# Performance work log

Measured on AMD Instinct MI355X. Metric: run time of the kernel, lower is better.

The kernel has to match this reference:

```python
import jax, jax.numpy as jnp
import numpy as np

N, E, D = 50000, 200000, 128   # graph nodes, graph edges (= line-graph nodes), feature dim
L = 2                          # number of GINEConv iterations (linegraph init arg)


def _build_line_graph(col0, col1):
    """Exact sparse equivalent of torch.nonzero((col1[:,None]==col0[None,:]) & (col0[:,None]!=col1[:,None])).
    Returns line edges (i -> j) with col1[i] == col0[j] and edge i not a self-loop,
    plus edge_attr_idx = col1[lg_src] (the shared graph node)."""
    order = np.argsort(col0, kind='stable')              # edges grouped by source node
    counts = np.bincount(col0, minlength=N)              # out-degree per node
    offsets = np.concatenate([[0], np.cumsum(counts)[:-1]])
    lengths = np.where(col0 != col1, counts[col1], 0)    # successors of each non-self-loop edge
    M = int(lengths.sum())
    lg_src = np.repeat(np.arange(E), lengths)
    cum = np.cumsum(lengths)
    pos = np.arange(M) - np.repeat(cum - lengths, lengths)  # position within each successor block
    lg_dst = order[np.repeat(offsets[col1], lengths) + pos]
    edge_attr_idx = col1[lg_src]
    return lg_src.astype(np.int64), lg_dst.astype(np.int64), edge_attr_idx.astype(np.int64)


def setup_inputs() -> dict:
    rng = np.random.RandomState(0)
    col0 = rng.randint(0, N, size=E).astype(np.int64)
    col1 = rng.randint(0, N, size=E).astype(np.int64)
    lg_src, lg_dst, edge_attr_idx = _build_line_graph(col0, col1)

    key = jax.random.key(0)
    kx, k1, k2 = jax.random.split(key, 3)
    scale = (2.0 / D) ** 0.5
    return {
        'x':  jax.random.normal(kx, (N, D), dtype=jnp.float32),
        'W1': jax.random.normal(k1, (D, D), dtype=jnp.float32) * scale,
        'b1': jnp.zeros((D,), dtype=jnp.float32),
        'W2': jax.random.normal(k2, (D, D), dtype=jnp.float32) * scale,
        'b2': jnp.zeros((D,), dtype=jnp.float32),
        'col0': jnp.asarray(col0),
        'col1': jnp.asarray(col1),
        'lg_src': jnp.asarray(lg_src),
        'lg_dst': jnp.asarray(lg_dst),
        'edge_attr_idx': jnp.asarray(edge_attr_idx),
    }


def reference(x, W1, b1, W2, b2, col0, col1, lg_src, lg_dst, edge_attr_idx):
    # line-graph node features: mean of endpoint features of each original edge
    lgX = 0.5 * (x[col0] + x[col1])                       # [E, D]
    lgE = x[edge_attr_idx]                                # [M, D] line-edge attrs (fixed across iterations)

    for _ in range(L):  # GINEConv, eps = 0 (PyG default)
        m = jax.nn.relu(lgX[lg_src] + lgE)                # [M, D] messages
        aggr = jax.ops.segment_sum(m, lg_dst, num_segments=E)  # scatter-add at target line-nodes
        h = lgX + aggr                                    # (1 + eps) * x + aggr
        lgX = jax.nn.relu(h @ W1 + b1) @ W2 + b2          # gin_nn MLP

    # scatter_mean back to graph nodes by col1 (zeros where no incident edge, matching pad)
    sums = jax.ops.segment_sum(lgX, col1, num_segments=N)                     # [N, D]
    cnt = jax.ops.segment_sum(jnp.ones((lgX.shape[0], 1), lgX.dtype), col1, num_segments=N)
    gx = jnp.where(cnt > 0, sums / jnp.maximum(cnt, 1.0), 0.0)

    out = jax.nn.relu(gx)
    # dropout p=0.0 -> identity; residual=True
    return x + out
```

## Files before the change

### kernel.cpp

```cpp
#include <hip/hip_runtime.h>
#include <hip/hip_bf16.h>

constexpr int NN = 50000;
constexpr int EE = 200000;
typedef __bf16 bf16x8 __attribute__((ext_vector_type(8)));
typedef float f32x4 __attribute__((ext_vector_type(4)));

__device__ __forceinline__ float b2f(unsigned short s) {
    union { unsigned u; float f; } c; c.u = ((unsigned)s) << 16; return c.f;
}
__device__ __forceinline__ unsigned short f2b(float f) {
    union { float f; unsigned u; } c; c.f = f;
    unsigned u = c.u + 0x7fffu + ((c.u >> 16) & 1u);
    return (unsigned short)(u >> 16);
}
__device__ __forceinline__ float xv(const void* p, long i, int f32m) {
    return f32m ? ((const float*)p)[i] : b2f(((const unsigned short*)p)[i]);
}
__device__ __forceinline__ int iv(const int* p, int i, int i64m) {
    return i64m ? p[2 * i] : p[i];
}

__global__ void k_detect(const unsigned short* x16, const int* c32, int* flg) {
    __shared__ int sf, si;
    int t = threadIdx.x;
    if (t == 0) { sf = 0; si = 1; }
    __syncthreads();
    for (int i = t; i < 16384; i += 256)
        if (((x16[i] >> 7) & 0xFF) == 0xFF) sf = 1;
    if (t < 64)
        if (c32[2 * t + 1] != 0) si = 0;
    __syncthreads();
    if (t == 0) { flg[0] = sf; flg[1] = si; }
}

__global__ void k_zero(unsigned* p, int n) {
    int i = blockIdx.x * 256 + threadIdx.x;
    if (i < n) p[i] = 0u;
}

__global__ void k_cast(const void* x, unsigned short* xb, const int* flg) {
    int i = blockIdx.x * 256 + threadIdx.x;
    if (i >= NN * 16) return;
    if (flg[0]) {
        const float4* xp = (const float4*)x + (size_t)i * 2;
        float4 u = xp[0], v = xp[1];
        unsigned short o[8] = { f2b(u.x), f2b(u.y), f2b(u.z), f2b(u.w),
                                f2b(v.x), f2b(v.y), f2b(v.z), f2b(v.w) };
        *(uint4*)(xb + (size_t)i * 8) = *(const uint4*)o;
    } else {
        ((uint4*)xb)[i] = ((const uint4*)x)[i];
    }
}

__global__ void k_wfrag(const void* W, unsigned short* Wf, const int* flg) {
    int f32m = flg[0];
    int chunk = blockIdx.x * 256 + threadIdx.x;
    if (chunk >= 2048) return;
    int l = chunk & 63, c = (chunk >> 6) & 3, t = chunk >> 8;
    int n = t * 16 + (l & 15), k0 = c * 32 + ((l >> 4) * 8);
    for (int j = 0; j < 8; j++) Wf[chunk * 8 + j] = f2b(xv(W, (long)(k0 + j) * 128 + n, f32m));
}

__global__ void k_hist(const int* col1, int* counts, const int* flg) {
    int e = blockIdx.x * 256 + threadIdx.x;
    if (e >= EE) return;
    atomicAdd(&counts[iv(col1, e, flg[1])], 1);
}

__global__ void k_scan1(const int* counts, int* bsum) {
    __shared__ int sh[256];
    int b = blockIdx.x, t = threadIdx.x;
    int idx = b * 256 + t;
    sh[t] = (idx < NN) ? counts[idx] : 0;
    __syncthreads();
    for (int off = 128; off > 0; off >>= 1) {
        if (t < off) sh[t] += sh[t + off];
        __syncthreads();
    }
    if (t == 0) bsum[b] = sh[0];
}

__global__ void k_scan2(const int* counts, const int* bsum,
                        int* row_ptr, int* cursor) {
    __shared__ int sh[256];
    __shared__ int base_s;
    int b = blockIdx.x, t = threadIdx.x;
    sh[t] = (t < b) ? bsum[t] : 0;
    __syncthreads();
    for (int off = 128; off > 0; off >>= 1) {
        if (t < off) sh[t] += sh[t + off];
        __syncthreads();
    }
    if (t == 0) base_s = sh[0];
    __syncthreads();
    int idx = b * 256 + t;
    int v = (idx < NN) ? counts[idx] : 0;
    sh[t] = v;
    __syncthreads();
    for (int off = 1; off < 256; off <<= 1) {
        int add = (t >= off) ? sh[t - off] : 0;
        __syncthreads();
        sh[t] += add;
        __syncthreads();
    }
    int ex = base_s + sh[t] - v;
    if (idx < NN) { row_ptr[idx] = ex; cursor[idx] = ex; }
    if (idx == NN - 1) row_ptr[NN] = ex + v;
}

__global__ void k_cscatter(const int* col0, const int* col1, int* cursor,
                           unsigned* aux, int* node1, const int* flg) {
    int e = blockIdx.x * 256 + threadIdx.x;
    if (e >= EE) return;
    int i64m = flg[1];
    int a = iv(col0, e, i64m), b = iv(col1, e, i64m);
    int pos = atomicAdd(&cursor[b], 1);
    aux[pos] = (unsigned)a | (a == b ? 0x80000000u : 0u);
    node1[pos] = b;
}

__global__ void k_gath(const unsigned short* xb, const unsigned short* lgX,
                       const int* row_ptr, const unsigned* aux,
                       unsigned short* S, int mode) {
    int n = blockIdx.x * 4 + (threadIdx.x >> 6);
    if (n >= NN) return;
    int l = threadIdx.x & 63, k0 = l * 2;
    int lo = row_ptr[n], hi = row_ptr[n + 1];
    unsigned un = *(const unsigned*)(xb + (size_t)n * 128 + k0);
    float xn0 = b2f((unsigned short)un), xn1 = b2f((unsigned short)(un >> 16));
    float a0 = 0.0f, a1 = 0.0f;
    if (mode == 1) {
        for (int p = lo; p < hi; p++) {
            unsigned av = aux[p];
            if (av & 0x80000000u) continue;
            unsigned u = *(const unsigned*)(xb + (size_t)av * 128 + k0);
            a0 += fmaxf(0.5f * b2f((unsigned short)u) + 1.5f * xn0, 0.0f);
            a1 += fmaxf(0.5f * b2f((unsigned short)(u >> 16)) + 1.5f * xn1, 0.0f);
        }
    } else {
        for (int p = lo; p < hi; p++) {
            if (aux[p] & 0x80000000u) continue;
            unsigned u = *(const unsigned*)(lgX + (size_t)p * 128 + k0);
            a0 += fmaxf(b2f((unsigned short)u) + xn0, 0.0f);
            a1 += fmaxf(b2f((unsigned short)(u >> 16)) + xn1, 0.0f);
        }
    }
    unsigned o = ((unsigned)f2b(a1) << 16) | (unsigned)f2b(a0);
    *(unsigned*)(S + (size_t)n * 128 + k0) = o;
}

__global__ __launch_bounds__(256, 8)
void k_fused(const unsigned short* A, const unsigned short* S,
             const unsigned* aux, const int* node1, const unsigned short* xb,
             const void* bias1, const void* bias2,
             const unsigned short* Wf1, const unsigned short* Wf2,
             unsigned short* Out, const int* flg, int initA) {
    __shared__ unsigned short Lds[8192];
    int f32m = flg[0];
    int tid = threadIdx.x;
    int w = tid >> 6, l = tid & 63;
    int lq = l >> 4, ln = l & 15;
    int e0 = blockIdx.x * 64 + w * 16;
    unsigned short* W_ = Lds + w * 2048;

    int row = e0 + ln;
    int aN = (int)(aux[row] & 0x7fffffffu);
    int bN = initA ? node1[row] : 0;
    for (int c = 0; c < 4; c++) {
        int k0 = c * 32 + lq * 8;
        uint4 svv = *(const uint4*)(S + (size_t)aN * 128 + k0);
        const unsigned short* sp = (const unsigned short*)&svv;
        unsigned short v[8];
        if (initA) {
            uint4 xav = *(const uint4*)(xb + (size_t)aN * 128 + k0);
            uint4 xbv = *(const uint4*)(xb + (size_t)bN * 128 + k0);
            const unsigned short* xa = (const unsigned short*)&xav;
            const unsigned short* xc = (const unsigned short*)&xbv;
            for (int j = 0; j < 8; j++)
                v[j] = f2b(0.5f * (b2f(xa[j]) + b2f(xc[j])) + b2f(sp[j]));
        } else {
            uint4 av = *(const uint4*)(A + (size_t)row * 128 + k0);
            const unsigned short* ap = (const unsigned short*)&av;
            for (int j = 0; j < 8; j++) v[j] = f2b(b2f(ap[j]) + b2f(sp[j]));
        }
        *(uint4*)(W_ + (c * 64 + l) * 8) = *(const uint4*)v;
    }

    f32x4 acc[8];
    for (int j = 0; j < 8; j++)
        for (int r = 0; r < 4; r++) acc[j][r] = 0.0f;
    for (int c = 0; c < 4; c++) {
        bf16x8 af = *(const bf16x8*)(W_ + (c * 64 + l) * 8);
        for (int j = 0; j < 8; j++) {
            bf16x8 bf = *(const bf16x8*)(Wf1 + (size_t)(((j * 4 + c) * 64 + l) * 8));
            acc[j] = __builtin_amdgcn_mfma_f32_16x16x32_bf16(af, bf, acc[j], 0, 0, 0);
        }
    }

    for (int j = 0; j < 8; j++) {
        int n = j * 16 + ln;
        float bv = xv(bias1, n, f32m);
        int c2 = n >> 5, lhi = ((n >> 3) & 3) * 16, j2 = n & 7;
        for (int rg = 0; rg < 4; rg++) {
            float h = acc[j][rg] + bv;
            if (h < 0.0f) h = 0.0f;
            W_[(c2 * 64 + lhi + lq * 4 + rg) * 8 + j2] = f2b(h);
        }
    }

    for (int j = 0; j < 8; j++)
        for (int r = 0; r < 4; r++) acc[j][r] = 0.0f;
    for (int c = 0; c < 4; c++) {
        bf16x8 af = *(const bf16x8*)(W_ + (c * 64 + l) * 8);
        for (int j = 0; j < 8; j++) {
            bf16x8 bf = *(const bf16x8*)(Wf2 + (size_t)(((j * 4 + c) * 64 + l) * 8));
            acc[j] = __builtin_amdgcn_mfma_f32_16x16x32_bf16(af, bf, acc[j], 0, 0, 0);
        }
    }

    for (int j = 0; j < 8; j++) {
        int n = j * 16 + ln;
        float bv = xv(bias2, n, f32m);
        for (int rg = 0; rg < 4; rg++)
            W_[(lq * 4 + rg) * 128 + n] = f2b(acc[j][rg] + bv);
    }
    for (int i = 0; i < 4; i++) {
        int idx = i * 64 + l;
        ((uint4*)Out)[(size_t)e0 * 16 + idx] = ((const uint4*)W_)[idx];
    }
}

__global__ void LGNNGINELayer_12463995093126_kernel(
    const void* x, const unsigned short* lgX, const int* row_ptr,
    void* out, const int* flg) {
    int n = blockIdx.x * 4 + (threadIdx.x >> 6);
    if (n >= NN) return;
    int l = threadIdx.x & 63, k0 = l * 2;
    int f32m = flg[0];
    int lo = row_ptr[n], hi = row_ptr[n + 1];
    float a0 = 0.0f, a1 = 0.0f;
    for (int p = lo; p < hi; p++) {
        unsigned u = *(const unsigned*)(lgX + (size_t)p * 128 + k0);
        a0 += b2f((unsigned short)u);
        a1 += b2f((unsigned short)(u >> 16));
    }
    float g0 = 0.0f, g1 = 0.0f;
    if (hi > lo) {
        float inv = 1.0f / (float)(hi - lo);
        g0 = fmaxf(a0 * inv, 0.0f);
        g1 = fmaxf(a1 * inv, 0.0f);
    }
    if (f32m) {
        ((float*)out)[(long)n * 128 + k0]     = ((const float*)x)[(long)n * 128 + k0] + g0;
        ((float*)out)[(long)n * 128 + k0 + 1] = ((const float*)x)[(long)n * 128 + k0 + 1] + g1;
    } else {
        unsigned u = *(const unsigned*)((const unsigned short*)x + (long)n * 128 + k0);
        float r0 = b2f((unsigned short)u) + g0;
        float r1 = b2f((unsigned short)(u >> 16)) + g1;
        unsigned o = ((unsigned)f2b(r1) << 16) | (unsigned)f2b(r0);
        *(unsigned*)((unsigned short*)out + (long)n * 128 + k0) = o;
    }
}

extern "C" void kernel_launch(void* const* d_in, const int* in_sizes, int n_in,
                              void* d_out, int out_size, void* d_ws, size_t ws_size,
                              hipStream_t stream) {
    (void)in_sizes; (void)n_in; (void)out_size; (void)ws_size;
    const void* x = d_in[0];
    const void* W1 = d_in[1];
    const void* b1 = d_in[2];
    const void* W2 = d_in[3];
    const void* b2 = d_in[4];
    const int* col0 = (const int*)d_in[5];
    const int* col1 = (const int*)d_in[6];

    char* p = (char*)d_ws;
    unsigned short* lgX = (unsigned short*)p; p += (size_t)EE * 128 * 2;
    unsigned short* S = (unsigned short*)p;   p += (size_t)NN * 128 * 2;
    unsigned short* xb = (unsigned short*)p;  p += (size_t)NN * 128 * 2;
    int* row_ptr = (int*)p;                   p += (size_t)(NN + 16) * 4;
    int* cursor = (int*)p;                    p += (size_t)NN * 4;
    int* counts = (int*)p;                    p += (size_t)NN * 4;
    int* bsum = (int*)p;                      p += 256 * 4;
    unsigned* aux = (unsigned*)p;             p += (size_t)EE * 4;
    int* node1 = (int*)p;                     p += (size_t)EE * 4;
    int* flg = (int*)p;                       p += 256;
    unsigned short* Wf1 = (unsigned short*)p; p += 16384 * 2;
    unsigned short* Wf2 = (unsigned short*)p;

    int gB = EE / 64;
    int eB = (EE + 255) / 256;
    int nB4 = (NN + 3) / 4;
    int sB = (NN + 255) / 256;
    int cB = (NN * 16 + 255) / 256;

    k_detect<<<1, 256, 0, stream>>>((const unsigned short*)x, col0, flg);
    k_cast<<<cB, 256, 0, stream>>>(x, xb, flg);
    k_wfrag<<<8, 256, 0, stream>>>(W1, Wf1, flg);
    k_wfrag<<<8, 256, 0, stream>>>(W2, Wf2, flg);

    k_zero<<<(NN + 255) / 256, 256, 0, stream>>>((unsigned*)counts, NN);
    k_hist<<<eB, 256, 0, stream>>>(col1, counts, flg);
    k_scan1<<<sB, 256, 0, stream>>>(counts, bsum);
    k_scan2<<<sB, 256, 0, stream>>>(counts, bsum, row_ptr, cursor);
    k_cscatter<<<eB, 256, 0, stream>>>(col0, col1, cursor, aux, node1, flg);

    k_gath<<<nB4, 256, 0, stream>>>(xb, lgX, row_ptr, aux, S, 1);
    k_fused<<<gB, 256, 0, stream>>>(lgX, S, aux, node1, xb, b1, b2,
                                    Wf1, Wf2, lgX, flg, 1);
    k_gath<<<nB4, 256, 0, stream>>>(xb, lgX, row_ptr, aux, S, 2);
    k_fused<<<gB, 256, 0, stream>>>(lgX, S, aux, node1, xb, b1, b2,
                                    Wf1, Wf2, lgX, flg, 0);
    LGNNGINELayer_12463995093126_kernel<<<nB4, 256, 0, stream>>>(
        x, lgX, row_ptr, d_out, flg);
}
```

Baseline: 383.0 us.

## Use hardware bf16 conversion, merge weight-fragment launches, keep A operand in registers

Replaces the manual round-to-nearest bf16 packing with native __bf16 casts and packed stores in several kernels. The two weight-fragment launches become one 16-block launch, and the counts zero kernel becomes hipMemsetAsync. In the fused MLP kernel the first GEMM's A fragments stay in registers instead of going through an LDS store and reload. These trim launch count and conversion instructions, at the cost of somewhat higher register pressure in the fused kernel.

```diff
diff --git a/kernel.cpp b/kernel.cpp
--- a/kernel.cpp
+++ b/kernel.cpp
@@ -9,6 +9,12 @@
 __device__ __forceinline__ float b2f(unsigned short s) {
     union { unsigned u; float f; } c; c.u = ((unsigned)s) << 16; return c.f;
 }
+__device__ __forceinline__ unsigned short bfbits(float f) {
+    union { __bf16 b; unsigned short u; } c; c.b = (__bf16)f; return c.u;
+}
+__device__ __forceinline__ unsigned pkbf(float lo, float hi) {
+    return ((unsigned)bfbits(hi) << 16) | bfbits(lo);
+}
 __device__ __forceinline__ unsigned short f2b(float f) {
     union { float f; unsigned u; } c; c.f = f;
     unsigned u = c.u + 0x7fffu + ((c.u >> 16) & 1u);
@@ -32,11 +38,6 @@
         if (c32[2 * t + 1] != 0) si = 0;
     __syncthreads();
     if (t == 0) { flg[0] = sf; flg[1] = si; }
-}
-
-__global__ void k_zero(unsigned* p, int n) {
-    int i = blockIdx.x * 256 + threadIdx.x;
-    if (i < n) p[i] = 0u;
 }
 
 __global__ void k_cast(const void* x, unsigned short* xb, const int* flg) {
@@ -45,21 +46,25 @@
     if (flg[0]) {
         const float4* xp = (const float4*)x + (size_t)i * 2;
         float4 u = xp[0], v = xp[1];
-        unsigned short o[8] = { f2b(u.x), f2b(u.y), f2b(u.z), f2b(u.w),
-                                f2b(v.x), f2b(v.y), f2b(v.z), f2b(v.w) };
-        *(uint4*)(xb + (size_t)i * 8) = *(const uint4*)o;
+        uint4 o;
+        o.x = pkbf(u.x, u.y); o.y = pkbf(u.z, u.w);
+        o.z = pkbf(v.x, v.y); o.w = pkbf(v.z, v.w);
+        ((uint4*)xb)[i] = o;
     } else {
         ((uint4*)xb)[i] = ((const uint4*)x)[i];
     }
 }
 
-__global__ void k_wfrag(const void* W, unsigned short* Wf, const int* flg) {
+__global__ void k_wfrag2(const void* W1, const void* W2,
+                         unsigned short* Wf1, unsigned short* Wf2, const int* flg) {
     int f32m = flg[0];
-    int chunk = blockIdx.x * 256 + threadIdx.x;
-    if (chunk >= 2048) return;
+    int g = blockIdx.x;
+    const void* W = (g < 8) ? W1 : W2;
+    unsigned short* Wf = (g < 8) ? Wf1 : Wf2;
+    int chunk = (g & 7) * 256 + threadIdx.x;
     int l = chunk & 63, c = (chunk >> 6) & 3, t = chunk >> 8;
     int n = t * 16 + (l & 15), k0 = c * 32 + ((l >> 4) * 8);
-    for (int j = 0; j < 8; j++) Wf[chunk * 8 + j] = f2b(xv(W, (long)(k0 + j) * 128 + n, f32m));
+    for (int j = 0; j < 8; j++) Wf[chunk * 8 + j] = bfbits(xv(W, (long)(k0 + j) * 128 + n, f32m));
 }
 
 __global__ void k_hist(const int* col1, int* counts, const int* flg) {
@@ -146,8 +151,7 @@
             a1 += fmaxf(b2f((unsigned short)(u >> 16)) + xn1, 0.0f);
         }
     }
-    unsigned o = ((unsigned)f2b(a1) << 16) | (unsigned)f2b(a0);
-    *(unsigned*)(S + (size_t)n * 128 + k0) = o;
+    *(unsigned*)(S + (size_t)n * 128 + k0) = pkbf(a0, a1);
 }
 
 __global__ __launch_bounds__(256, 8)
@@ -167,34 +171,33 @@
     int row = e0 + ln;
     int aN = (int)(aux[row] & 0x7fffffffu);
     int bN = initA ? node1[row] : 0;
+    bf16x8 af[4];
     for (int c = 0; c < 4; c++) {
         int k0 = c * 32 + lq * 8;
         uint4 svv = *(const uint4*)(S + (size_t)aN * 128 + k0);
         const unsigned short* sp = (const unsigned short*)&svv;
-        unsigned short v[8];
         if (initA) {
             uint4 xav = *(const uint4*)(xb + (size_t)aN * 128 + k0);
             uint4 xbv = *(const uint4*)(xb + (size_t)bN * 128 + k0);
             const unsigned short* xa = (const unsigned short*)&xav;
             const unsigned short* xc = (const unsigned short*)&xbv;
             for (int j = 0; j < 8; j++)
-                v[j] = f2b(0.5f * (b2f(xa[j]) + b2f(xc[j])) + b2f(sp[j]));
+                af[c][j] = (__bf16)(0.5f * (b2f(xa[j]) + b2f(xc[j])) + b2f(sp[j]));
         } else {
             uint4 av = *(const uint4*)(A + (size_t)row * 128 + k0);
             const unsigned short* ap = (const unsigned short*)&av;
-            for (int j = 0; j < 8; j++) v[j] = f2b(b2f(ap[j]) + b2f(sp[j]));
-        }
-        *(uint4*)(W_ + (c * 64 + l) * 8) = *(const uint4*)v;
+            for (int j = 0; j < 8; j++)
+                af[c][j] = (__bf16)(b2f(ap[j]) + b2f(sp[j]));
+        }
     }
 
     f32x4 acc[8];
     for (int j = 0; j < 8; j++)
         for (int r = 0; r < 4; r++) acc[j][r] = 0.0f;
     for (int c = 0; c < 4; c++) {
-        bf16x8 af = *(const bf16x8*)(W_ + (c * 64 + l) * 8);
         for (int j = 0; j < 8; j++) {
             bf16x8 bf = *(const bf16x8*)(Wf1 + (size_t)(((j * 4 + c) * 64 + l) * 8));
-            acc[j] = __builtin_amdgcn_mfma_f32_16x16x32_bf16(af, bf, acc[j], 0, 0, 0);
+            acc[j] = __builtin_amdgcn_mfma_f32_16x16x32_bf16(af[c], bf, acc[j], 0, 0, 0);
         }
     }
 
@@ -203,19 +206,18 @@
         float bv = xv(bias1, n, f32m);
         int c2 = n >> 5, lhi = ((n >> 3) & 3) * 16, j2 = n & 7;
         for (int rg = 0; rg < 4; rg++) {
-            float h = acc[j][rg] + bv;
-            if (h < 0.0f) h = 0.0f;
-            W_[(c2 * 64 + lhi + lq * 4 + rg) * 8 + j2] = f2b(h);
+            float h = fmaxf(acc[j][rg] + bv, 0.0f);
+            W_[(c2 * 64 + lhi + lq * 4 + rg) * 8 + j2] = bfbits(h);
         }
     }
 
     for (int j = 0; j < 8; j++)
         for (int r = 0; r < 4; r++) acc[j][r] = 0.0f;
     for (int c = 0; c < 4; c++) {
-        bf16x8 af = *(const bf16x8*)(W_ + (c * 64 + l) * 8);
+        bf16x8 a2 = *(const bf16x8*)(W_ + (c * 64 + l) * 8);
         for (int j = 0; j < 8; j++) {
             bf16x8 bf = *(const bf16x8*)(Wf2 + (size_t)(((j * 4 + c) * 64 + l) * 8));
-            acc[j] = __builtin_amdgcn_mfma_f32_16x16x32_bf16(af, bf, acc[j], 0, 0, 0);
+            acc[j] = __builtin_amdgcn_mfma_f32_16x16x32_bf16(a2, bf, acc[j], 0, 0, 0);
         }
     }
 
@@ -223,7 +225,7 @@
         int n = j * 16 + ln;
         float bv = xv(bias2, n, f32m);
         for (int rg = 0; rg < 4; rg++)
-            W_[(lq * 4 + rg) * 128 + n] = f2b(acc[j][rg] + bv);
+            W_[(lq * 4 + rg) * 128 + n] = bfbits(acc[j][rg] + bv);
     }
     for (int i = 0; i < 4; i++) {
         int idx = i * 64 + l;
@@ -258,8 +260,7 @@
         unsigned u = *(const unsigned*)((const unsigned short*)x + (long)n * 128 + k0);
         float r0 = b2f((unsigned short)u) + g0;
         float r1 = b2f((unsigned short)(u >> 16)) + g1;
-        unsigned o = ((unsigned)f2b(r1) << 16) | (unsigned)f2b(r0);
-        *(unsigned*)((unsigned short*)out + (long)n * 128 + k0) = o;
+        *(unsigned*)((unsigned short*)out + (long)n * 128 + k0) = pkbf(r0, r1);
     }
 }
 
@@ -297,10 +298,9 @@
 
     k_detect<<<1, 256, 0, stream>>>((const unsigned short*)x, col0, flg);
     k_cast<<<cB, 256, 0, stream>>>(x, xb, flg);
-    k_wfrag<<<8, 256, 0, stream>>>(W1, Wf1, flg);
-    k_wfrag<<<8, 256, 0, stream>>>(W2, Wf2, flg);
-
-    k_zero<<<(NN + 255) / 256, 256, 0, stream>>>((unsigned*)counts, NN);
+    k_wfrag2<<<16, 256, 0, stream>>>(W1, W2, Wf1, Wf2, flg);
+
+    hipMemsetAsync(counts, 0, (size_t)NN * 4, stream);
     k_hist<<<eB, 256, 0, stream>>>(col1, counts, flg);
     k_scan1<<<sB, 256, 0, stream>>>(counts, bsum);
     k_scan2<<<sB, 256, 0, stream>>>(counts, bsum, row_ptr, cursor);
```

Result: no change. 385.2 us (+0.6%).
